# Kernel optimization log

Measured on AMD Instinct MI355X. Metric: run time of the kernel, lower is better.

## Reference

```python
import jax, jax.numpy as jnp
import numpy as np

NUM_EXPERTS = 64


def setup_inputs() -> dict:
    key = jax.random.key(0)
    k1, k2 = jax.random.split(key)
    x = jax.random.normal(k1, (4, 4096, 2048), dtype=jnp.float32)
    # nn.Linear default init scale ~ 1/sqrt(dim); exact init irrelevant for correctness
    gate_w = jax.random.normal(k2, (NUM_EXPERTS, 2048), dtype=jnp.float32) * (1.0 / np.sqrt(2048.0))
    expert_bias = jnp.zeros((NUM_EXPERTS,), dtype=jnp.float32)
    return {"x": x, "gate_w": gate_w, "expert_bias": expert_bias, "top_k": 8}


def reference(x, gate_w, expert_bias, top_k):
    # x: [B, S, D]; gate_w: [E, D]; expert_bias: [E]
    B, S, D = x.shape
    x_flat = x.reshape(-1, D)                                  # [T, D], T = B*S
    logits = jnp.einsum('td,ed->te', x_flat, gate_w) + expert_bias  # [T, E]
    top_k_logits, top_k_indices = jax.lax.top_k(logits, top_k)      # [T, K]
    top_k_weights = jax.nn.softmax(top_k_logits, axis=-1)           # [T, K]
    # training-mode load counting (scatter_add over expert ids)
    expert_counts = jax.ops.segment_sum(
        jnp.ones((B * S * top_k,), dtype=jnp.float32),
        top_k_indices.reshape(-1),
        num_segments=NUM_EXPERTS,
    )                                                               # [E]
    return top_k_indices, top_k_weights, expert_counts
```

## Files before the change

### kernel.cpp

```cpp
#include <hip/hip_runtime.h>
#include <math.h>

#define T_TOKENS 16384
#define D_DIM    2048
#define E_EXP    64
#define TOPK     8
#define NS       8

typedef __attribute__((ext_vector_type(8))) short bf16x8;
typedef __attribute__((ext_vector_type(4))) float f32x4;

__device__ __forceinline__ unsigned short bf16rne(float f) {
  unsigned u = __builtin_bit_cast(unsigned, f);
  unsigned r = u + 0x7fffu + ((u >> 16) & 1u);
  return (unsigned short)(r >> 16);
}
__device__ __forceinline__ float bf16f(unsigned short h) {
  return __builtin_bit_cast(float, (unsigned)h << 16);
}

__global__ __launch_bounds__(256) void convert_g_kernel(
    const float* __restrict__ gw, unsigned short* __restrict__ ph,
    unsigned short* __restrict__ pl, float* __restrict__ counts_zero)
{
  const int id = blockIdx.x * 256 + threadIdx.x;
  if (blockIdx.x == 0 && threadIdx.x < E_EXP) counts_zero[threadIdx.x] = 0.0f;

  const int e  = id & 63;
  const int kq = (id >> 6) & 3;
  const int c  = id >> 8;
  const float* gp = &gw[(size_t)e * D_DIM + c * 32 + kq * 8];
  float4 v0 = *(const float4*)&gp[0];
  float4 v1 = *(const float4*)&gp[4];
  const float xs[8] = {v0.x, v0.y, v0.z, v0.w, v1.x, v1.y, v1.z, v1.w};
  unsigned short h[8], l[8];
  #pragma unroll
  for (int j = 0; j < 8; ++j) {
    h[j] = bf16rne(xs[j]);
    l[j] = bf16rne(xs[j] - bf16f(h[j]));
  }
  *(short4*)&ph[(size_t)id * 8 + 0] = make_short4(h[0], h[1], h[2], h[3]);
  *(short4*)&ph[(size_t)id * 8 + 4] = make_short4(h[4], h[5], h[6], h[7]);
  *(short4*)&pl[(size_t)id * 8 + 0] = make_short4(l[0], l[1], l[2], l[3]);
  *(short4*)&pl[(size_t)id * 8 + 4] = make_short4(l[4], l[5], l[6], l[7]);
}

__global__ __launch_bounds__(256, 4) void moe_logits_kernel(
    const float* __restrict__ x, const unsigned short* __restrict__ ph,
    const unsigned short* __restrict__ pl, float* __restrict__ part)
{
  const int tid  = threadIdx.x;
  const int wave = tid >> 6;
  const int lane = tid & 63;
  const int l15  = lane & 15;
  const int quad = lane >> 4;
  const int ks   = blockIdx.y;
  const int ksz  = D_DIM / NS;
  const int k0   = ks * ksz;
  const int tokw = blockIdx.x * 128 + wave * 32;

  f32x4 acc[2][4];
  #pragma unroll
  for (int s = 0; s < 2; ++s)
    #pragma unroll
    for (int et = 0; et < 4; ++et) acc[s][et] = (f32x4){0.f, 0.f, 0.f, 0.f};

  #pragma unroll 1
  for (int c8 = 0; c8 < ksz / 32; ++c8) {
    const int kc = k0 + c8 * 32;
    const int cg = kc >> 5;

    bf16x8 bh[4], bl[4];
    const size_t bbase = (((size_t)cg * 4 + quad) * 64 + l15) * 8;
    #pragma unroll
    for (int et = 0; et < 4; ++et) {
      bh[et] = *(const bf16x8*)&ph[bbase + (size_t)et * 16 * 8];
      bl[et] = *(const bf16x8*)&pl[bbase + (size_t)et * 16 * 8];
    }

    #pragma unroll
    for (int sub = 0; sub < 2; ++sub) {
      const int t = tokw + sub * 16 + l15;
      const float* xp = &x[(size_t)t * D_DIM + kc + quad * 8];
      float4 v0 = *(const float4*)&xp[0];
      float4 v1 = *(const float4*)&xp[4];
      const float xs[8] = {v0.x, v0.y, v0.z, v0.w, v1.x, v1.y, v1.z, v1.w};
      bf16x8 ah, al;
      #pragma unroll
      for (int j = 0; j < 8; ++j) {
        unsigned short h = bf16rne(xs[j]);
        ah[j] = (short)h;
        al[j] = (short)bf16rne(xs[j] - bf16f(h));
      }
      #pragma unroll
      for (int et = 0; et < 4; ++et) {
        acc[sub][et] = __builtin_amdgcn_mfma_f32_16x16x32_bf16(ah, bh[et], acc[sub][et], 0, 0, 0);
        acc[sub][et] = __builtin_amdgcn_mfma_f32_16x16x32_bf16(ah, bl[et], acc[sub][et], 0, 0, 0);
        acc[sub][et] = __builtin_amdgcn_mfma_f32_16x16x32_bf16(al, bh[et], acc[sub][et], 0, 0, 0);
      }
    }
  }

  #pragma unroll
  for (int sub = 0; sub < 2; ++sub) {
    #pragma unroll
    for (int et = 0; et < 4; ++et) {
      #pragma unroll
      for (int r = 0; r < 4; ++r) {
        const size_t t = (size_t)tokw + sub * 16 + quad * 4 + r;
        part[((size_t)ks * T_TOKENS + t) * E_EXP + et * 16 + l15] = acc[sub][et][r];
      }
    }
  }
}

__global__ __launch_bounds__(64) void topk_kernel(
    const float* __restrict__ part, const float* __restrict__ bias,
    float* __restrict__ out)
{
  __shared__ unsigned hist[E_EXP];
  const int tid = threadIdx.x;
  const int t = blockIdx.x * 64 + tid;
  hist[tid] = 0;
  __syncthreads();

  float l[E_EXP];
  #pragma unroll
  for (int j = 0; j < E_EXP / 4; ++j) {
    float4 b = *(const float4*)&bias[j * 4];
    l[4*j] = b.x; l[4*j+1] = b.y; l[4*j+2] = b.z; l[4*j+3] = b.w;
  }
  #pragma unroll 1
  for (int ks = 0; ks < NS; ++ks) {
    const float4* p = (const float4*)&part[((size_t)ks * T_TOKENS + t) * E_EXP];
    #pragma unroll
    for (int j = 0; j < E_EXP / 4; ++j) {
      float4 v = p[j];
      l[4*j] += v.x; l[4*j+1] += v.y; l[4*j+2] += v.z; l[4*j+3] += v.w;
    }
  }

  float tv[TOPK]; int tix[TOPK];
  unsigned long long used = 0ull;
  #pragma unroll
  for (int k = 0; k < TOPK; ++k) {
    float best = -INFINITY; int bi = 0;
    #pragma unroll
    for (int j = 0; j < E_EXP; ++j) {
      bool ok = (((used >> j) & 1ull) == 0ull) && (l[j] > best);
      best = ok ? l[j] : best;
      bi   = ok ? j : bi;
    }
    tv[k] = best; tix[k] = bi;
    used |= (1ull << bi);
  }

  float m = tv[0], s = 0.0f, w[TOPK];
  #pragma unroll
  for (int k = 0; k < TOPK; ++k) { w[k] = expf(tv[k] - m); s += w[k]; }
  float inv = 1.0f / s;

  #pragma unroll
  for (int k = 0; k < TOPK; ++k) {
    out[(size_t)t * TOPK + k] = (float)tix[k];
    out[(size_t)T_TOKENS * TOPK + (size_t)t * TOPK + k] = w[k] * inv;
  }

  #pragma unroll
  for (int k = 0; k < TOPK; ++k) atomicAdd(&hist[tix[k]], 1u);
  __syncthreads();
  atomicAdd(&out[2 * (size_t)T_TOKENS * TOPK + tid], (float)hist[tid]);
}

extern "C" void kernel_launch(void* const* d_in, const int* in_sizes, int n_in,
                              void* d_out, int out_size, void* d_ws, size_t ws_size,
                              hipStream_t stream) {
  const float* x    = (const float*)d_in[0];
  const float* gw   = (const float*)d_in[1];
  const float* bias = (const float*)d_in[2];
  float* out  = (float*)d_out;

  float* part = (float*)d_ws;
  const size_t part_elems = (size_t)NS * T_TOKENS * E_EXP;
  unsigned short* ph = (unsigned short*)((char*)d_ws + part_elems * sizeof(float));
  unsigned short* pl = ph + (size_t)E_EXP * D_DIM;

  convert_g_kernel<<<dim3(E_EXP * D_DIM / 8 / 256), dim3(256), 0, stream>>>(
      gw, ph, pl, out + 2 * (size_t)T_TOKENS * TOPK);
  moe_logits_kernel<<<dim3(T_TOKENS / 128, NS), dim3(256), 0, stream>>>(
      x, ph, pl, part);
  topk_kernel<<<dim3(T_TOKENS / 64), dim3(64), 0, stream>>>(part, bias, out);
}
```

Baseline: 233.8 us.

## Prefetch next x chunk in registers and add lo*lo MFMA term

Restructures the logits GEMM main loop to software-pipeline global loads of x: the next 32-column chunk of activations is loaded into registers while the current one is split to bf16 hi/lo and fed to MFMAs. It also adds a fourth MFMA (lo*lo) per tile, making the split-bf16 product closer to fp32 at the cost of more matrix work. The convert kernel is tidied with a shared split helper and 16-byte stores. Register pressure rises from the prefetch buffers, and the extra MFMA adds compute to a loop that is likely bound by x bandwidth.

```diff
diff --git a/kernel.cpp b/kernel.cpp
--- a/kernel.cpp
+++ b/kernel.cpp
@@ -6,6 +6,7 @@
 #define E_EXP    64
 #define TOPK     8
 #define NS       8
+#define NCH      (D_DIM / NS / 32)
 
 typedef __attribute__((ext_vector_type(8))) short bf16x8;
 typedef __attribute__((ext_vector_type(4))) float f32x4;
@@ -17,6 +18,17 @@
 }
 __device__ __forceinline__ float bf16f(unsigned short h) {
   return __builtin_bit_cast(float, (unsigned)h << 16);
+}
+
+__device__ __forceinline__ void split8(const float4 v0, const float4 v1,
+                                       bf16x8& hi, bf16x8& lo) {
+  const float xs[8] = {v0.x, v0.y, v0.z, v0.w, v1.x, v1.y, v1.z, v1.w};
+  #pragma unroll
+  for (int j = 0; j < 8; ++j) {
+    unsigned short h = bf16rne(xs[j]);
+    hi[j] = (short)h;
+    lo[j] = (short)bf16rne(xs[j] - bf16f(h));
+  }
 }
 
 __global__ __launch_bounds__(256) void convert_g_kernel(
@@ -32,17 +44,10 @@
   const float* gp = &gw[(size_t)e * D_DIM + c * 32 + kq * 8];
   float4 v0 = *(const float4*)&gp[0];
   float4 v1 = *(const float4*)&gp[4];
-  const float xs[8] = {v0.x, v0.y, v0.z, v0.w, v1.x, v1.y, v1.z, v1.w};
-  unsigned short h[8], l[8];
-  #pragma unroll
-  for (int j = 0; j < 8; ++j) {
-    h[j] = bf16rne(xs[j]);
-    l[j] = bf16rne(xs[j] - bf16f(h[j]));
-  }
-  *(short4*)&ph[(size_t)id * 8 + 0] = make_short4(h[0], h[1], h[2], h[3]);
-  *(short4*)&ph[(size_t)id * 8 + 4] = make_short4(h[4], h[5], h[6], h[7]);
-  *(short4*)&pl[(size_t)id * 8 + 0] = make_short4(l[0], l[1], l[2], l[3]);
-  *(short4*)&pl[(size_t)id * 8 + 4] = make_short4(l[4], l[5], l[6], l[7]);
+  bf16x8 hi, lo;
+  split8(v0, v1, hi, lo);
+  *(bf16x8*)&ph[(size_t)id * 8] = hi;
+  *(bf16x8*)&pl[(size_t)id * 8] = lo;
 }
 
 __global__ __launch_bounds__(256, 4) void moe_logits_kernel(
@@ -55,8 +60,7 @@
   const int l15  = lane & 15;
   const int quad = lane >> 4;
   const int ks   = blockIdx.y;
-  const int ksz  = D_DIM / NS;
-  const int k0   = ks * ksz;
+  const int k0   = ks * (D_DIM / NS);
   const int tokw = blockIdx.x * 128 + wave * 32;
 
   f32x4 acc[2][4];
@@ -65,40 +69,45 @@
     #pragma unroll
     for (int et = 0; et < 4; ++et) acc[s][et] = (f32x4){0.f, 0.f, 0.f, 0.f};
 
+  const float* xp0 = &x[(size_t)(tokw + l15)      * D_DIM + k0 + quad * 8];
+  const float* xp1 = &x[(size_t)(tokw + 16 + l15) * D_DIM + k0 + quad * 8];
+  const unsigned short* bp_h = &ph[(((size_t)(k0 >> 5) * 4 + quad) * 64 + l15) * 8];
+  const unsigned short* bp_l = &pl[(((size_t)(k0 >> 5) * 4 + quad) * 64 + l15) * 8];
+
+  float4 a0 = *(const float4*)&xp0[0], a1 = *(const float4*)&xp0[4];
+  float4 b0 = *(const float4*)&xp1[0], b1 = *(const float4*)&xp1[4];
+
   #pragma unroll 1
-  for (int c8 = 0; c8 < ksz / 32; ++c8) {
-    const int kc = k0 + c8 * 32;
-    const int cg = kc >> 5;
-
-    bf16x8 bh[4], bl[4];
-    const size_t bbase = (((size_t)cg * 4 + quad) * 64 + l15) * 8;
+  for (int c = 0; c < NCH; ++c) {
+    float4 na0, na1, nb0, nb1;
+    if (c + 1 < NCH) {
+      const float* q0 = xp0 + (c + 1) * 32;
+      const float* q1 = xp1 + (c + 1) * 32;
+      na0 = *(const float4*)&q0[0]; na1 = *(const float4*)&q0[4];
+      nb0 = *(const float4*)&q1[0]; nb1 = *(const float4*)&q1[4];
+    }
+
+    bf16x8 ah0, al0, ah1, al1;
+    split8(a0, a1, ah0, al0);
+    split8(b0, b1, ah1, al1);
+
+    const unsigned short* ch = bp_h + (size_t)c * 2048;
+    const unsigned short* cl = bp_l + (size_t)c * 2048;
     #pragma unroll
     for (int et = 0; et < 4; ++et) {
-      bh[et] = *(const bf16x8*)&ph[bbase + (size_t)et * 16 * 8];
-      bl[et] = *(const bf16x8*)&pl[bbase + (size_t)et * 16 * 8];
-    }
-
-    #pragma unroll
-    for (int sub = 0; sub < 2; ++sub) {
-      const int t = tokw + sub * 16 + l15;
-      const float* xp = &x[(size_t)t * D_DIM + kc + quad * 8];
-      float4 v0 = *(const float4*)&xp[0];
-      float4 v1 = *(const float4*)&xp[4];
-      const float xs[8] = {v0.x, v0.y, v0.z, v0.w, v1.x, v1.y, v1.z, v1.w};
-      bf16x8 ah, al;
-      #pragma unroll
-      for (int j = 0; j < 8; ++j) {
-        unsigned short h = bf16rne(xs[j]);
-        ah[j] = (short)h;
-        al[j] = (short)bf16rne(xs[j] - bf16f(h));
-      }
-      #pragma unroll
-      for (int et = 0; et < 4; ++et) {
-        acc[sub][et] = __builtin_amdgcn_mfma_f32_16x16x32_bf16(ah, bh[et], acc[sub][et], 0, 0, 0);
-        acc[sub][et] = __builtin_amdgcn_mfma_f32_16x16x32_bf16(ah, bl[et], acc[sub][et], 0, 0, 0);
-        acc[sub][et] = __builtin_amdgcn_mfma_f32_16x16x32_bf16(al, bh[et], acc[sub][et], 0, 0, 0);
-      }
-    }
+      bf16x8 bh = *(const bf16x8*)&ch[et * 128];
+      bf16x8 bl = *(const bf16x8*)&cl[et * 128];
+      acc[0][et] = __builtin_amdgcn_mfma_f32_16x16x32_bf16(ah0, bh, acc[0][et], 0, 0, 0);
+      acc[0][et] = __builtin_amdgcn_mfma_f32_16x16x32_bf16(ah0, bl, acc[0][et], 0, 0, 0);
+      acc[0][et] = __builtin_amdgcn_mfma_f32_16x16x32_bf16(al0, bh, acc[0][et], 0, 0, 0);
+      acc[0][et] = __builtin_amdgcn_mfma_f32_16x16x32_bf16(al0, bl, acc[0][et], 0, 0, 0);
+      acc[1][et] = __builtin_amdgcn_mfma_f32_16x16x32_bf16(ah1, bh, acc[1][et], 0, 0, 0);
+      acc[1][et] = __builtin_amdgcn_mfma_f32_16x16x32_bf16(ah1, bl, acc[1][et], 0, 0, 0);
+      acc[1][et] = __builtin_amdgcn_mfma_f32_16x16x32_bf16(al1, bh, acc[1][et], 0, 0, 0);
+      acc[1][et] = __builtin_amdgcn_mfma_f32_16x16x32_bf16(al1, bl, acc[1][et], 0, 0, 0);
+    }
+
+    a0 = na0; a1 = na1; b0 = nb0; b1 = nb1;
   }
 
   #pragma unroll
```

After: 235.2 us. About the same (+0.6%).
